# Kernel optimization log

Measured on AMD Instinct MI355X. Metric: run time of the kernel, lower is better.

The kernel has to match this reference:

```python
import jax, jax.numpy as jnp
import numpy as np

N_P = 100000   # number of platforms (rows of pF)
N_M = 100000   # number of modules (rows of M)
R = 64         # embedding rank r = M.shape[1]
S = 3          # number of interference terms s
B = 500000     # batch of (i, j, k) index triples
ALPHA = 0.001
BETA = 0.001


def setup_inputs() -> dict:
    key = jax.random.key(0)
    k1, k2, k3 = jax.random.split(key, 3)
    pF = jax.random.normal(k1, (N_P, R * (1 + 2 * S)), dtype=jnp.float32)
    M = jax.random.normal(k2, (N_M, R), dtype=jnp.float32)
    ijk = jax.random.randint(k3, (B, 3), 0, N_M)  # i,j,k indices; k==-1 would mask
    return {"pF": pF, "M": M, "ijk": ijk}


def reference(pF, M, ijk):
    # MatrixFactorizationIF.__call__ with baseline=None, full=False, log=True.
    r = M.shape[1]
    i, j, k = ijk[:, 0], ijk[:, 1], ijk[:, 2]
    pFi = pF[i]                                        # [B, r*(1+2s)] gather
    Pi = pFi[:, :r]                                    # [B, r]
    Vs = BETA * pFi[:, r:(1 + S) * r].reshape(-1, r, S)  # [B, r, s]
    Vg = BETA * pFi[:, (1 + S) * r:].reshape(-1, r, S)   # [B, r, s]
    Mj = M[j]                                          # [B, r]
    kc = jnp.where(k < 0, 0, k)                        # clamp invalid k for gather
    Mk = M[kc]                                         # [B, r]
    mask = (k != -1).astype(M.dtype)                   # 1[valid k]
    a = jnp.einsum('brs,br->bs', Vs, Mj)               # V_s[i]^T m_j
    g = jnp.einsum('brs,br->bs', Vg, Mk)               # V_g[i]^T m_k
    mFm = mask * jnp.sum(a * g, axis=-1)               # interference term
    return ALPHA * jnp.sum(Pi * Mj, axis=-1) + mFm     # C_bar = 0 (no baseline)
```

## Files before the change

### kernel.cpp

```cpp
#include <hip/hip_runtime.h>

constexpr float ALPHA = 0.001f;
constexpr float BETA  = 0.001f;
constexpr int R   = 64;
constexpr int S   = 3;
constexpr int PFW = R * (1 + 2 * S);
constexpr int BSH  = 7;
constexpr int MAXB = 800;
constexpr int SBLK = 256;
constexpr int RCAP = 1536;

__device__ __forceinline__ float bfhi(unsigned u) {
    union { unsigned u; float f; } c; c.u = u & 0xffff0000u; return c.f;
}
__device__ __forceinline__ float bflo(unsigned u) {
    union { unsigned u; float f; } c; c.u = u << 16; return c.f;
}

__global__ __launch_bounds__(256) void convM_kernel(const float* __restrict__ M,
                                                    uint4* __restrict__ Mb, int n8) {
    int idx = blockIdx.x * 256 + threadIdx.x;
    if (idx >= n8) return;
    const float4* src = reinterpret_cast<const float4*>(M);
    float4 a = src[2 * idx], b = src[2 * idx + 1];
    union { float f; unsigned u; } c;
    unsigned w[8];
    c.f = a.x; w[0] = c.u; c.f = a.y; w[1] = c.u; c.f = a.z; w[2] = c.u; c.f = a.w; w[3] = c.u;
    c.f = b.x; w[4] = c.u; c.f = b.y; w[5] = c.u; c.f = b.z; w[6] = c.u; c.f = b.w; w[7] = c.u;
    #pragma unroll
    for (int t = 0; t < 8; ++t) w[t] = (w[t] + 0x7fffu + ((w[t] >> 16) & 1u)) >> 16;
    Mb[idx] = make_uint4(w[0] | (w[1] << 16), w[2] | (w[3] << 16),
                         w[4] | (w[5] << 16), w[6] | (w[7] << 16));
}

__global__ __launch_bounds__(256) void hist_kernel(const int* __restrict__ ijk, int B,
                                                   int chunk, int nb, int* __restrict__ hist) {
    __shared__ int lh[MAXB];
    for (int t = threadIdx.x; t < nb; t += blockDim.x) lh[t] = 0;
    __syncthreads();
    const int lo = blockIdx.x * chunk, hi = min(B, lo + chunk);
    for (int idx = lo + threadIdx.x; idx < hi; idx += blockDim.x)
        atomicAdd(&lh[ijk[3 * idx] >> BSH], 1);
    __syncthreads();
    for (int t = threadIdx.x; t < nb; t += blockDim.x)
        if (lh[t]) atomicAdd(&hist[t], lh[t]);
}

__global__ __launch_bounds__(1024) void scan_kernel(const int* __restrict__ hist,
                                                    int* __restrict__ offs,
                                                    int* __restrict__ cursor, int nb) {
    __shared__ int buf[1024];
    int t = threadIdx.x;
    int own = (t < nb) ? hist[t] : 0;
    buf[t] = own;
    __syncthreads();
    for (int d = 1; d < 1024; d <<= 1) {
        int v = (t >= d) ? buf[t - d] : 0;
        __syncthreads();
        buf[t] += v;
        __syncthreads();
    }
    if (t < nb) { int e = buf[t] - own; offs[t] = e; cursor[t] = e; }
}

__global__ __launch_bounds__(256) void scatter_kernel(const int* __restrict__ ijk, int B,
                                                      int chunk, int nb,
                                                      int* __restrict__ cursor,
                                                      int4* __restrict__ sorted) {
    __shared__ int cnt[MAXB];
    __shared__ int base[MAXB];
    __shared__ int rnk[MAXB];
    for (int t = threadIdx.x; t < nb; t += blockDim.x) { cnt[t] = 0; rnk[t] = 0; }
    __syncthreads();
    const int lo = blockIdx.x * chunk, hi = min(B, lo + chunk);
    for (int idx = lo + threadIdx.x; idx < hi; idx += blockDim.x)
        atomicAdd(&cnt[ijk[3 * idx] >> BSH], 1);
    __syncthreads();
    for (int t = threadIdx.x; t < nb; t += blockDim.x)
        if (cnt[t]) base[t] = atomicAdd(&cursor[t], cnt[t]);
    __syncthreads();
    for (int idx = lo + threadIdx.x; idx < hi; idx += blockDim.x) {
        const int i = ijk[3 * idx], j = ijk[3 * idx + 1], k = ijk[3 * idx + 2];
        const int bkt = i >> BSH;
        const int p = base[bkt] + atomicAdd(&rnk[bkt], 1);
        sorted[p] = make_int4(i, j, k, idx);
    }
}

__global__ __launch_bounds__(256) void refine_kernel(int4* __restrict__ sorted,
                                                     const int* __restrict__ offs,
                                                     int B, int nb) {
    const int bkt = blockIdx.x;
    const int start = offs[bkt];
    const int end = (bkt + 1 < nb) ? offs[bkt + 1] : B;
    const int count = end - start;
    if (count <= 1 || count > RCAP) return;

    __shared__ int4 ent[RCAP];
    __shared__ int cnt[128];
    __shared__ int base[128];

    for (int t = threadIdx.x; t < 128; t += 256) cnt[t] = 0;
    __syncthreads();
    for (int t = threadIdx.x; t < count; t += 256) {
        int4 e = sorted[start + t];
        ent[t] = e;
        atomicAdd(&cnt[e.x & 127], 1);
    }
    __syncthreads();
    if (threadIdx.x == 0) {
        int run = 0;
        #pragma unroll 4
        for (int t = 0; t < 128; ++t) { base[t] = run; run += cnt[t]; }
    }
    __syncthreads();
    for (int t = threadIdx.x; t < 128; t += 256) cnt[t] = 0;
    __syncthreads();
    for (int t = threadIdx.x; t < count; t += 256) {
        int4 e = ent[t];
        const int key = e.x & 127;
        const int p = base[key] + atomicAdd(&cnt[key], 1);
        sorted[start + p] = e;
    }
}

__global__ __launch_bounds__(256) void mf_if_kernel(
    const float* __restrict__ pF,
    const float* __restrict__ M,
    const uint2* __restrict__ Mb,
    const int4*  __restrict__ sorted,
    const int*   __restrict__ ijk,
    float* __restrict__ out,
    int B, int nwg)
{
    const int orig = blockIdx.x;
    const int q = nwg >> 3, r = nwg & 7;
    const int xcd = orig & 7;
    const int wgid = (xcd < r ? xcd * (q + 1) : r * (q + 1) + (xcd - r) * q) + (orig >> 3);

    const int sub = threadIdx.x & 15;
    const long pos = (long)wgid * 16 + (threadIdx.x >> 4);
    if (pos >= B) return;

    int4 s;
    if (sorted) s = sorted[pos];
    else s = make_int4(ijk[3 * pos], ijk[3 * pos + 1], ijk[3 * pos + 2], (int)pos);

    const int kc = (s.z < 0) ? 0 : s.z;

    const float4* pFi = reinterpret_cast<const float4*>(pF + (size_t)s.x * PFW);

    float4 mj, mk;
    if (Mb) {
        const uint2 uj = Mb[(size_t)s.y * 16 + sub];
        const uint2 uk = Mb[(size_t)kc  * 16 + sub];
        mj = make_float4(bflo(uj.x), bfhi(uj.x), bflo(uj.y), bfhi(uj.y));
        mk = make_float4(bflo(uk.x), bfhi(uk.x), bflo(uk.y), bfhi(uk.y));
    } else {
        mj = reinterpret_cast<const float4*>(M + (size_t)s.y * R)[sub];
        mk = reinterpret_cast<const float4*>(M + (size_t)kc  * R)[sub];
    }

    const float4 pi = pFi[sub];
    float p = pi.x * mj.x + pi.y * mj.y + pi.z * mj.z + pi.w * mj.w;

    const float4 v0 = pFi[16 + 3 * sub + 0];
    const float4 v1 = pFi[16 + 3 * sub + 1];
    const float4 v2 = pFi[16 + 3 * sub + 2];
    float a0 = v0.x * mj.x + v0.w * mj.y + v1.z * mj.z + v2.y * mj.w;
    float a1 = v0.y * mj.x + v1.x * mj.y + v1.w * mj.z + v2.z * mj.w;
    float a2 = v0.z * mj.x + v1.y * mj.y + v2.x * mj.z + v2.w * mj.w;

    const float4 w0 = pFi[64 + 3 * sub + 0];
    const float4 w1 = pFi[64 + 3 * sub + 1];
    const float4 w2 = pFi[64 + 3 * sub + 2];
    float g0 = w0.x * mk.x + w0.w * mk.y + w1.z * mk.z + w2.y * mk.w;
    float g1 = w0.y * mk.x + w1.x * mk.y + w1.w * mk.z + w2.z * mk.w;
    float g2 = w0.z * mk.x + w1.y * mk.y + w2.x * mk.z + w2.w * mk.w;

    #pragma unroll
    for (int off = 8; off >= 1; off >>= 1) {
        p  += __shfl_xor(p,  off);
        a0 += __shfl_xor(a0, off);
        a1 += __shfl_xor(a1, off);
        a2 += __shfl_xor(a2, off);
        g0 += __shfl_xor(g0, off);
        g1 += __shfl_xor(g1, off);
        g2 += __shfl_xor(g2, off);
    }

    if (sub == 0) {
        const float mfm = (s.z != -1)
            ? (BETA * BETA) * (a0 * g0 + a1 * g1 + a2 * g2) : 0.0f;
        out[s.w] = ALPHA * p + mfm;
    }
}

extern "C" void kernel_launch(void* const* d_in, const int* in_sizes, int n_in,
                              void* d_out, int out_size, void* d_ws, size_t ws_size,
                              hipStream_t stream) {
    const float* pF  = (const float*)d_in[0];
    const float* M   = (const float*)d_in[1];
    const int*   ijk = (const int*)d_in[2];
    float* out = (float*)d_out;

    const int B   = in_sizes[2] / 3;
    const int N_P = in_sizes[0] / PFW;
    const int N_M = in_sizes[1] / R;
    const int nb  = (N_P + (1 << BSH) - 1) >> BSH;

    const size_t sorted_off = 16 * 1024;
    const size_t mb_off     = sorted_off + (size_t)B * sizeof(int4);
    const size_t need_sort  = mb_off;
    const size_t need_full  = mb_off + (size_t)N_M * R * 2;

    int4*  sorted = nullptr;
    uint2* Mb     = nullptr;

    if (nb <= MAXB && ws_size >= need_sort) {
        int* hist   = (int*)d_ws;
        int* offs   = hist + 1024;
        int* cursor = hist + 2048;
        sorted = (int4*)((char*)d_ws + sorted_off);
        const int chunk = (B + SBLK - 1) / SBLK;

        hipMemsetAsync(hist, 0, 1024 * sizeof(int), stream);
        hist_kernel<<<SBLK, 256, 0, stream>>>(ijk, B, chunk, nb, hist);
        scan_kernel<<<1, 1024, 0, stream>>>(hist, offs, cursor, nb);
        scatter_kernel<<<SBLK, 256, 0, stream>>>(ijk, B, chunk, nb, cursor, sorted);
        refine_kernel<<<nb, 256, 0, stream>>>(sorted, offs, B, nb);
    }
    if (ws_size >= need_full) {
        Mb = (uint2*)((char*)d_ws + mb_off);
        const int n8 = N_M * R / 8;
        convM_kernel<<<(n8 + 255) / 256, 256, 0, stream>>>(M, (uint4*)Mb, n8);
    }

    const int nwg = (B + 15) / 16;
    mf_if_kernel<<<nwg, 256, 0, stream>>>(pF, M, Mb, sorted, ijk, out, B, nwg);
}
```

Before: 98.05 us.

## Process sorted runs of entries per group to reuse pF row registers

The main kernel now has each 16-lane group handle 8 consecutive sorted entries, staged through shared memory. It prefetches all Mj/Mk bf16 rows up front and reloads the pF row only when the platform index changes, so runs of repeated indices reuse registers. The M-to-bf16 conversion now uses nontemporal loads, and the unsorted fallback is split into a separate kernel. The cost is more registers per thread, fewer workgroups, and serialized per-entry shuffle reductions within each group.

Result: slower. 112.6 us (+14.9%).

```diff
diff --git a/kernel.cpp b/kernel.cpp
--- a/kernel.cpp
+++ b/kernel.cpp
@@ -9,6 +9,8 @@
 constexpr int MAXB = 800;
 constexpr int SBLK = 256;
 constexpr int RCAP = 1536;
+constexpr int GE   = 8;
+constexpr int EPB  = 16 * GE;
 
 __device__ __forceinline__ float bfhi(unsigned u) {
     union { unsigned u; float f; } c; c.u = u & 0xffff0000u; return c.f;
@@ -21,14 +23,14 @@
                                                     uint4* __restrict__ Mb, int n8) {
     int idx = blockIdx.x * 256 + threadIdx.x;
     if (idx >= n8) return;
-    const float4* src = reinterpret_cast<const float4*>(M);
-    float4 a = src[2 * idx], b = src[2 * idx + 1];
-    union { float f; unsigned u; } c;
+    const float* src = M + (size_t)idx * 8;
     unsigned w[8];
-    c.f = a.x; w[0] = c.u; c.f = a.y; w[1] = c.u; c.f = a.z; w[2] = c.u; c.f = a.w; w[3] = c.u;
-    c.f = b.x; w[4] = c.u; c.f = b.y; w[5] = c.u; c.f = b.z; w[6] = c.u; c.f = b.w; w[7] = c.u;
-    #pragma unroll
-    for (int t = 0; t < 8; ++t) w[t] = (w[t] + 0x7fffu + ((w[t] >> 16) & 1u)) >> 16;
+    #pragma unroll
+    for (int t = 0; t < 8; ++t) {
+        union { float f; unsigned u; } c;
+        c.f = __builtin_nontemporal_load(src + t);
+        w[t] = (c.u + 0x7fffu + ((c.u >> 16) & 1u)) >> 16;
+    }
     Mb[idx] = make_uint4(w[0] | (w[1] << 16), w[2] | (w[3] << 16),
                          w[4] | (w[5] << 16), w[6] | (w[7] << 16));
 }
@@ -124,12 +126,10 @@
     }
 }
 
-__global__ __launch_bounds__(256) void mf_if_kernel(
+__global__ __launch_bounds__(256) void mf_if_run_kernel(
     const float* __restrict__ pF,
-    const float* __restrict__ M,
     const uint2* __restrict__ Mb,
     const int4*  __restrict__ sorted,
-    const int*   __restrict__ ijk,
     float* __restrict__ out,
     int B, int nwg)
 {
@@ -138,42 +138,98 @@
     const int xcd = orig & 7;
     const int wgid = (xcd < r ? xcd * (q + 1) : r * (q + 1) + (xcd - r) * q) + (orig >> 3);
 
+    __shared__ int4 ents[EPB];
+    const long blkbase = (long)wgid * EPB;
+    if (threadIdx.x < EPB) {
+        const long p = blkbase + threadIdx.x;
+        ents[threadIdx.x] = (p < B) ? sorted[p] : make_int4(-1, 0, 0, 0);
+    }
+    __syncthreads();
+
     const int sub = threadIdx.x & 15;
-    const long pos = (long)wgid * 16 + (threadIdx.x >> 4);
+    const int eb  = (threadIdx.x >> 4) * GE;
+
+    uint2 uj[GE], uk[GE];
+    #pragma unroll
+    for (int e = 0; e < GE; ++e) {
+        const int4 s = ents[eb + e];
+        const int jj = (s.x < 0) ? 0 : s.y;
+        const int kk = (s.x < 0 || s.z < 0) ? 0 : s.z;
+        uj[e] = Mb[(size_t)jj * 16 + sub];
+        uk[e] = Mb[(size_t)kk * 16 + sub];
+    }
+
+    float4 pi, v0, v1, v2, w0, w1, w2;
+    int cur = -2;
+
+    #pragma unroll
+    for (int e = 0; e < GE; ++e) {
+        const int4 s = ents[eb + e];
+        if (s.x < 0) continue;
+        if (s.x != cur) {
+            const float4* pFi = reinterpret_cast<const float4*>(pF + (size_t)s.x * PFW);
+            pi = pFi[sub];
+            v0 = pFi[16 + 3 * sub]; v1 = pFi[17 + 3 * sub]; v2 = pFi[18 + 3 * sub];
+            w0 = pFi[64 + 3 * sub]; w1 = pFi[65 + 3 * sub]; w2 = pFi[66 + 3 * sub];
+            cur = s.x;
+        }
+        const float4 mj = make_float4(bflo(uj[e].x), bfhi(uj[e].x),
+                                      bflo(uj[e].y), bfhi(uj[e].y));
+        const float4 mk = make_float4(bflo(uk[e].x), bfhi(uk[e].x),
+                                      bflo(uk[e].y), bfhi(uk[e].y));
+
+        float p  = pi.x * mj.x + pi.y * mj.y + pi.z * mj.z + pi.w * mj.w;
+        float a0 = v0.x * mj.x + v0.w * mj.y + v1.z * mj.z + v2.y * mj.w;
+        float a1 = v0.y * mj.x + v1.x * mj.y + v1.w * mj.z + v2.z * mj.w;
+        float a2 = v0.z * mj.x + v1.y * mj.y + v2.x * mj.z + v2.w * mj.w;
+        float g0 = w0.x * mk.x + w0.w * mk.y + w1.z * mk.z + w2.y * mk.w;
+        float g1 = w0.y * mk.x + w1.x * mk.y + w1.w * mk.z + w2.z * mk.w;
+        float g2 = w0.z * mk.x + w1.y * mk.y + w2.x * mk.z + w2.w * mk.w;
+
+        #pragma unroll
+        for (int off = 8; off >= 1; off >>= 1) {
+            p  += __shfl_xor(p,  off);
+            a0 += __shfl_xor(a0, off);
+            a1 += __shfl_xor(a1, off);
+            a2 += __shfl_xor(a2, off);
+            g0 += __shfl_xor(g0, off);
+            g1 += __shfl_xor(g1, off);
+            g2 += __shfl_xor(g2, off);
+        }
+
+        if (sub == 0) {
+            const float mfm = (s.z != -1)
+                ? (BETA * BETA) * (a0 * g0 + a1 * g1 + a2 * g2) : 0.0f;
+            out[s.w] = ALPHA * p + mfm;
+        }
+    }
+}
+
+__global__ __launch_bounds__(256) void mf_if_kernel(
+    const float* __restrict__ pF,
+    const float* __restrict__ M,
+    const int*   __restrict__ ijk,
+    float* __restrict__ out,
+    int B)
+{
+    const int sub = threadIdx.x & 15;
+    const long pos = (long)blockIdx.x * 16 + (threadIdx.x >> 4);
     if (pos >= B) return;
 
-    int4 s;
-    if (sorted) s = sorted[pos];
-    else s = make_int4(ijk[3 * pos], ijk[3 * pos + 1], ijk[3 * pos + 2], (int)pos);
-
-    const int kc = (s.z < 0) ? 0 : s.z;
-
-    const float4* pFi = reinterpret_cast<const float4*>(pF + (size_t)s.x * PFW);
-
-    float4 mj, mk;
-    if (Mb) {
-        const uint2 uj = Mb[(size_t)s.y * 16 + sub];
-        const uint2 uk = Mb[(size_t)kc  * 16 + sub];
-        mj = make_float4(bflo(uj.x), bfhi(uj.x), bflo(uj.y), bfhi(uj.y));
-        mk = make_float4(bflo(uk.x), bfhi(uk.x), bflo(uk.y), bfhi(uk.y));
-    } else {
-        mj = reinterpret_cast<const float4*>(M + (size_t)s.y * R)[sub];
-        mk = reinterpret_cast<const float4*>(M + (size_t)kc  * R)[sub];
-    }
+    const int i = ijk[3 * pos], j = ijk[3 * pos + 1], k = ijk[3 * pos + 2];
+    const int kc = (k < 0) ? 0 : k;
+
+    const float4* pFi = reinterpret_cast<const float4*>(pF + (size_t)i * PFW);
+    const float4 mj = reinterpret_cast<const float4*>(M + (size_t)j  * R)[sub];
+    const float4 mk = reinterpret_cast<const float4*>(M + (size_t)kc * R)[sub];
 
     const float4 pi = pFi[sub];
     float p = pi.x * mj.x + pi.y * mj.y + pi.z * mj.z + pi.w * mj.w;
-
-    const float4 v0 = pFi[16 + 3 * sub + 0];
-    const float4 v1 = pFi[16 + 3 * sub + 1];
-    const float4 v2 = pFi[16 + 3 * sub + 2];
+    const float4 v0 = pFi[16 + 3 * sub], v1 = pFi[17 + 3 * sub], v2 = pFi[18 + 3 * sub];
     float a0 = v0.x * mj.x + v0.w * mj.y + v1.z * mj.z + v2.y * mj.w;
     float a1 = v0.y * mj.x + v1.x * mj.y + v1.w * mj.z + v2.z * mj.w;
     float a2 = v0.z * mj.x + v1.y * mj.y + v2.x * mj.z + v2.w * mj.w;
-
-    const float4 w0 = pFi[64 + 3 * sub + 0];
-    const float4 w1 = pFi[64 + 3 * sub + 1];
-    const float4 w2 = pFi[64 + 3 * sub + 2];
+    const float4 w0 = pFi[64 + 3 * sub], w1 = pFi[65 + 3 * sub], w2 = pFi[66 + 3 * sub];
     float g0 = w0.x * mk.x + w0.w * mk.y + w1.z * mk.z + w2.y * mk.w;
     float g1 = w0.y * mk.x + w1.x * mk.y + w1.w * mk.z + w2.z * mk.w;
     float g2 = w0.z * mk.x + w1.y * mk.y + w2.x * mk.z + w2.w * mk.w;
@@ -181,18 +237,12 @@
     #pragma unroll
     for (int off = 8; off >= 1; off >>= 1) {
         p  += __shfl_xor(p,  off);
-        a0 += __shfl_xor(a0, off);
-        a1 += __shfl_xor(a1, off);
-        a2 += __shfl_xor(a2, off);
-        g0 += __shfl_xor(g0, off);
-        g1 += __shfl_xor(g1, off);
-        g2 += __shfl_xor(g2, off);
-    }
-
+        a0 += __shfl_xor(a0, off); a1 += __shfl_xor(a1, off); a2 += __shfl_xor(a2, off);
+        g0 += __shfl_xor(g0, off); g1 += __shfl_xor(g1, off); g2 += __shfl_xor(g2, off);
+    }
     if (sub == 0) {
-        const float mfm = (s.z != -1)
-            ? (BETA * BETA) * (a0 * g0 + a1 * g1 + a2 * g2) : 0.0f;
-        out[s.w] = ALPHA * p + mfm;
+        const float mfm = (k != -1) ? (BETA * BETA) * (a0 * g0 + a1 * g1 + a2 * g2) : 0.0f;
+        out[pos] = ALPHA * p + mfm;
     }
 }
 
@@ -211,17 +261,14 @@
 
     const size_t sorted_off = 16 * 1024;
     const size_t mb_off     = sorted_off + (size_t)B * sizeof(int4);
-    const size_t need_sort  = mb_off;
     const size_t need_full  = mb_off + (size_t)N_M * R * 2;
 
-    int4*  sorted = nullptr;
-    uint2* Mb     = nullptr;
-
-    if (nb <= MAXB && ws_size >= need_sort) {
+    if (nb <= MAXB && ws_size >= need_full) {
         int* hist   = (int*)d_ws;
         int* offs   = hist + 1024;
         int* cursor = hist + 2048;
-        sorted = (int4*)((char*)d_ws + sorted_off);
+        int4*  sorted = (int4*)((char*)d_ws + sorted_off);
+        uint2* Mb     = (uint2*)((char*)d_ws + mb_off);
         const int chunk = (B + SBLK - 1) / SBLK;
 
         hipMemsetAsync(hist, 0, 1024 * sizeof(int), stream);
@@ -229,13 +276,13 @@
         scan_kernel<<<1, 1024, 0, stream>>>(hist, offs, cursor, nb);
         scatter_kernel<<<SBLK, 256, 0, stream>>>(ijk, B, chunk, nb, cursor, sorted);
         refine_kernel<<<nb, 256, 0, stream>>>(sorted, offs, B, nb);
-    }
-    if (ws_size >= need_full) {
-        Mb = (uint2*)((char*)d_ws + mb_off);
+
         const int n8 = N_M * R / 8;
         convM_kernel<<<(n8 + 255) / 256, 256, 0, stream>>>(M, (uint4*)Mb, n8);
-    }
-
-    const int nwg = (B + 15) / 16;
-    mf_if_kernel<<<nwg, 256, 0, stream>>>(pF, M, Mb, sorted, ijk, out, B, nwg);
-}
+
+        const int nwg = (B + EPB - 1) / EPB;
+        mf_if_run_kernel<<<nwg, 256, 0, stream>>>(pF, Mb, sorted, out, B, nwg);
+    } else {
+        mf_if_kernel<<<(B + 15) / 16, 256, 0, stream>>>(pF, M, ijk, out, B);
+    }
+}
```
